# Optimization experiments

Hardware: AMD Instinct MI355X
Metric: run time of the kernel (lower is better)

## Reference

```python
import jax, jax.numpy as jnp
import numpy as np

HEADS = 8
DIM_HEAD = 64
QUERY_DIM = 512
CONTEXT_DIM = 512
OUT_DIM = 512
INNER = HEADS * DIM_HEAD  # 512


def setup_inputs() -> dict:
    key = jax.random.key(0)
    ks = jax.random.split(key, 6)
    B, N, S, M = 2, 1024, 4, 2048
    x = jax.random.normal(ks[0], (B, N, S, QUERY_DIM), dtype=jnp.float32)
    context = jax.random.normal(ks[1], (B, M, CONTEXT_DIM), dtype=jnp.float32)
    # Linear weights stored as [in, out] so y = x @ W (matches torch Linear with W.T)
    Wq = jax.random.normal(ks[2], (QUERY_DIM, INNER), dtype=jnp.float32) / np.sqrt(QUERY_DIM)
    Wkv = jax.random.normal(ks[3], (CONTEXT_DIM, 2 * INNER), dtype=jnp.float32) / np.sqrt(CONTEXT_DIM)
    Wo = jax.random.normal(ks[4], (INNER, OUT_DIM), dtype=jnp.float32) / np.sqrt(INNER)
    bo = jax.random.normal(ks[5], (OUT_DIM,), dtype=jnp.float32) * 0.01
    return {"x": x, "context": context, "Wq": Wq, "Wkv": Wkv, "Wo": Wo, "bo": bo}


def reference(x, context, Wq, Wkv, Wo, bo):
    B, N, S, _ = x.shape
    M = context.shape[1]
    scale = DIM_HEAD ** -0.5
    # projections
    q = (x @ Wq).reshape(B, N, S, HEADS, DIM_HEAD)            # b n s h d
    kv = context @ Wkv                                        # b m (2*inner)
    k, v = jnp.split(kv, 2, axis=-1)
    k = k.reshape(B, M, HEADS, DIM_HEAD)                      # b m h d
    v = v.reshape(B, M, HEADS, DIM_HEAD)
    # attention scores: [(b h) s n m] expressed as bhsnm
    sim = jnp.einsum('bnshd,bmhd->bhsnm', q, k) * scale
    attn = jax.nn.softmax(sim, axis=-1)
    out = jnp.einsum('bhsnm,bmhd->bnshd', attn, v)            # b n s h d
    out = out.reshape(B, N, S, INNER)
    return out @ Wo + bo
```

## Files before the change

kernel.cpp:

```cpp
#include <hip/hip_runtime.h>

typedef __bf16 bf16;
typedef __bf16 bf16x8 __attribute__((ext_vector_type(8)));
typedef __bf16 bf16x4 __attribute__((ext_vector_type(4)));
typedef float f32x4 __attribute__((ext_vector_type(4)));

#define SCL 0.18033688011112042f

#define GLOAD_LDS16(g, l)                                          \
  __builtin_amdgcn_global_load_lds(                                \
      (const __attribute__((address_space(1))) void*)(g),          \
      (__attribute__((address_space(3))) void*)(l), 16, 0, 0)

__global__ __launch_bounds__(256) void convert_bf16(const float* __restrict__ x,
                                                    const float* __restrict__ ctx,
                                                    bf16* __restrict__ xb,
                                                    bf16* __restrict__ cb) {
  const int bid = blockIdx.x;
  const float* src;
  bf16* dst;
  size_t off;
  if (bid < 2048) { src = x; dst = xb; off = (size_t)bid * 2048; }
  else            { src = ctx; dst = cb; off = (size_t)(bid - 2048) * 2048; }
  size_t i = off + (size_t)threadIdx.x * 8;
  float4 a0 = *(const float4*)&src[i];
  float4 a1 = *(const float4*)&src[i + 4];
  bf16x8 o;
  o[0] = (bf16)a0.x; o[1] = (bf16)a0.y; o[2] = (bf16)a0.z; o[3] = (bf16)a0.w;
  o[4] = (bf16)a1.x; o[5] = (bf16)a1.y; o[6] = (bf16)a1.z; o[7] = (bf16)a1.w;
  *(bf16x8*)&dst[i] = o;
}

__global__ __launch_bounds__(256) void transpose_all(const float* __restrict__ Wq,
                                                     const float* __restrict__ Wkv,
                                                     const float* __restrict__ Wo,
                                                     bf16* __restrict__ Wqt,
                                                     bf16* __restrict__ Wkvt,
                                                     bf16* __restrict__ Wot) {
  __shared__ float tile[32][33];
  const int bx = blockIdx.x;
  const float* W; bf16* Wt; int N, n0;
  if (bx < 16)      { W = Wq;  Wt = Wqt;  N = 512;  n0 = bx * 32; }
  else if (bx < 48) { W = Wkv; Wt = Wkvt; N = 1024; n0 = (bx - 16) * 32; }
  else              { W = Wo;  Wt = Wot;  N = 512;  n0 = (bx - 48) * 32; }
  const int K = 512;
  const int tid = threadIdx.x;
  const int j = tid & 31, i0 = tid >> 5;
  const int k0 = blockIdx.y * 32;
#pragma unroll
  for (int ii = 0; ii < 4; ii++) {
    int i = i0 * 4 + ii;
    tile[i][j] = W[(size_t)(k0 + i) * N + n0 + j];
  }
  __syncthreads();
#pragma unroll
  for (int ii = 0; ii < 4; ii++) {
    int i = i0 * 4 + ii;
    Wt[(size_t)(n0 + i) * K + k0 + j] = (bf16)tile[j][i];
  }
}

template <int MODE>
__global__ __launch_bounds__(256) void gemm128(const bf16* __restrict__ A,
                                               const bf16* __restrict__ Bt,
                                               void* __restrict__ Cout,
                                               const float* __restrict__ bias,
                                               bf16* __restrict__ Vtb,
                                               int M, int N, int K) {
  const int tid = threadIdx.x;
  const int wave = tid >> 6, lane = tid & 63;
  const int quad = lane >> 4, l15 = lane & 15;
  const int m0 = blockIdx.y * 128, n0 = blockIdx.x * 128;

  __shared__ __align__(16) bf16 As[128 * 64];
  __shared__ __align__(16) bf16 Bs[128 * 64];

  f32x4 acc[4][4] = {};

  const int srow8 = lane >> 3, schunk = lane & 7;
  const int gchunk = schunk ^ srow8;
  const bf16* Ag = A + (size_t)(m0 + wave * 8 + srow8) * K + gchunk * 8;
  const bf16* Bg = Bt + (size_t)(n0 + wave * 8 + srow8) * K + gchunk * 8;
  bf16* Asw = &As[wave * 8 * 64];
  bf16* Bsw = &Bs[wave * 8 * 64];

  const int mrow = (wave & 1) * 64, ncol = (wave >> 1) * 64;

  for (int kt = 0; kt < K; kt += 64) {
#pragma unroll
    for (int r = 0; r < 4; r++) {
      GLOAD_LDS16(Ag + kt + (size_t)(r * 32) * K, Asw + r * 32 * 64);
      GLOAD_LDS16(Bg + kt + (size_t)(r * 32) * K, Bsw + r * 32 * 64);
    }
    __syncthreads();
#pragma unroll
    for (int h = 0; h < 2; h++) {
      bf16x8 af[4], bfr[4];
#pragma unroll
      for (int i = 0; i < 4; i++) {
        int R = mrow + i * 16 + l15;
        af[i] = *(const bf16x8*)&As[R * 64 + (((h * 4 + quad) ^ (R & 7)) * 8)];
      }
#pragma unroll
      for (int j = 0; j < 4; j++) {
        int R = ncol + j * 16 + l15;
        bfr[j] = *(const bf16x8*)&Bs[R * 64 + (((h * 4 + quad) ^ (R & 7)) * 8)];
      }
#pragma unroll
      for (int i = 0; i < 4; i++)
#pragma unroll
        for (int j = 0; j < 4; j++)
          acc[i][j] = __builtin_amdgcn_mfma_f32_16x16x32_bf16(af[i], bfr[j], acc[i][j], 0, 0, 0);
    }
    __syncthreads();
  }

#pragma unroll
  for (int i = 0; i < 4; i++) {
    const int row = m0 + mrow + i * 16 + quad * 4;
#pragma unroll
    for (int j = 0; j < 4; j++) {
      const int col = n0 + ncol + j * 16 + l15;
      if constexpr (MODE == 0) {
        bf16* C = (bf16*)Cout;
#pragma unroll
        for (int r = 0; r < 4; r++)
          C[(size_t)(row + r) * N + col] = (bf16)(acc[i][j][r] * SCL);
      } else if constexpr (MODE == 1) {
        if (col < 512) {
          bf16* Kb = (bf16*)Cout;
#pragma unroll
          for (int r = 0; r < 4; r++)
            Kb[(size_t)(row + r) * 512 + col] = (bf16)acc[i][j][r];
        } else {
          const int hh = (col - 512) >> 6, d = (col - 512) & 63;
          const int bb = row >> 11, mb = row & 2047;
          bf16x4 pk;
          pk[0] = (bf16)acc[i][j][0]; pk[1] = (bf16)acc[i][j][1];
          pk[2] = (bf16)acc[i][j][2]; pk[3] = (bf16)acc[i][j][3];
          *(bf16x4*)&Vtb[((size_t)(bb * 8 + hh) * 64 + d) * 2048 + mb] = pk;
        }
      } else {
        float* C = (float*)Cout;
        const float bv = bias[col];
#pragma unroll
        for (int r = 0; r < 4; r++)
          C[(size_t)(row + r) * N + col] = acc[i][j][r] + bv;
      }
    }
  }
}

__global__ __launch_bounds__(256) void attn_kernel(const bf16* __restrict__ q,
                                                   const bf16* __restrict__ Kb,
                                                   const bf16* __restrict__ Vtb,
                                                   bf16* __restrict__ attn_out) {
  const int tid = threadIdx.x;
  const int wave = tid >> 6, lane = tid & 63;
  const int quad = lane >> 4, l15 = lane & 15;
  const int bid = blockIdx.x;
  const int nt = bid & 15, h = (bid >> 4) & 7, s = (bid >> 7) & 3, b = bid >> 9;
  const int n0 = nt * 64;

  __shared__ __align__(16) bf16 Kl[2][64 * 64];
  __shared__ __align__(16) bf16 Vl[2][64 * 64];
  __shared__ __align__(16) bf16 Pl[4][16 * 64];
  bf16* Pw = &Pl[wave][0];

  const int nrow = n0 + wave * 16 + l15;
  const size_t qoff = ((size_t)((b * 1024 + nrow) * 4 + s)) * 512 + h * 64;
  const bf16x8 qf0 = *(const bf16x8*)&q[qoff + quad * 8];
  const bf16x8 qf1 = *(const bf16x8*)&q[qoff + 32 + quad * 8];

  float l_part = 0.0f;
  f32x4 o[4] = {};

  const int srow = tid >> 2, c0 = tid & 3;
  const bf16* Kg = Kb + (size_t)(b * 2048 + srow) * 512 + h * 64 + c0 * 16;
  const bf16* Vg = Vtb + ((size_t)(b * 8 + h) * 64 + srow) * 2048 + c0 * 16;
  const int ssw = srow & 7;
  const int koff0 = srow * 64 + ((c0 * 2) ^ ssw) * 8;
  const int koff1 = srow * 64 + ((c0 * 2 + 1) ^ ssw) * 8;

  uint4 kr0 = *(const uint4*)Kg;
  uint4 kr1 = *(const uint4*)(Kg + 8);
  uint4 vr0 = *(const uint4*)Vg;
  uint4 vr1 = *(const uint4*)(Vg + 8);
  *(uint4*)&Kl[0][koff0] = kr0; *(uint4*)&Kl[0][koff1] = kr1;
  *(uint4*)&Vl[0][koff0] = vr0; *(uint4*)&Vl[0][koff1] = vr1;

  const int psw = l15 & 7;

  for (int t = 0; t < 32; ++t) {
    __syncthreads();
    if (t < 31) {
      const bf16* kg = Kg + (size_t)(t + 1) * 64 * 512;
      const bf16* vg = Vg + (t + 1) * 64;
      kr0 = *(const uint4*)kg; kr1 = *(const uint4*)(kg + 8);
      vr0 = *(const uint4*)vg; vr1 = *(const uint4*)(vg + 8);
    }
    const bf16* Kc = &Kl[t & 1][0];
    const bf16* Vc = &Vl[t & 1][0];

    f32x4 sf[4];
#pragma unroll
    for (int mc = 0; mc < 4; mc++) {
      f32x4 z = {};
      bf16x8 kf0 = *(const bf16x8*)&Kc[(mc * 16 + l15) * 64 + ((quad ^ psw) * 8)];
      bf16x8 kf1 = *(const bf16x8*)&Kc[(mc * 16 + l15) * 64 + (((4 + quad) ^ psw) * 8)];
      z = __builtin_amdgcn_mfma_f32_16x16x32_bf16(kf0, qf0, z, 0, 0, 0);
      z = __builtin_amdgcn_mfma_f32_16x16x32_bf16(kf1, qf1, z, 0, 0, 0);
      sf[mc] = z;
    }

    float p[4][4];
#pragma unroll
    for (int mc = 0; mc < 4; mc++)
#pragma unroll
      for (int r = 0; r < 4; r++) {
        p[mc][r] = __builtin_amdgcn_exp2f(sf[mc][r]);
        l_part += p[mc][r];
      }

#pragma unroll
    for (int mc = 0; mc < 4; mc++) {
      bf16x4 pk;
      pk[0] = (bf16)p[mc][0]; pk[1] = (bf16)p[mc][1];
      pk[2] = (bf16)p[mc][2]; pk[3] = (bf16)p[mc][3];
      *(bf16x4*)&Pw[l15 * 64 + (((mc * 2 + (quad >> 1)) ^ psw)) * 8 + (quad & 1) * 4] = pk;
    }

#pragma unroll
    for (int mch = 0; mch < 2; mch++) {
      bf16x8 pf = *(const bf16x8*)&Pw[l15 * 64 + (((mch * 4 + quad) ^ psw)) * 8];
#pragma unroll
      for (int dg = 0; dg < 4; dg++) {
        bf16x8 vf = *(const bf16x8*)&Vc[(dg * 16 + l15) * 64 + (((mch * 4 + quad) ^ psw)) * 8];
        o[dg] = __builtin_amdgcn_mfma_f32_16x16x32_bf16(vf, pf, o[dg], 0, 0, 0);
      }
    }

    if (t < 31) {
      bf16* Kn = &Kl[(t + 1) & 1][0];
      bf16* Vn = &Vl[(t + 1) & 1][0];
      *(uint4*)&Kn[koff0] = kr0; *(uint4*)&Kn[koff1] = kr1;
      *(uint4*)&Vn[koff0] = vr0; *(uint4*)&Vn[koff1] = vr1;
    }
  }

  l_part += __shfl_xor(l_part, 16);
  l_part += __shfl_xor(l_part, 32);
  const float inv = 1.0f / l_part;
#pragma unroll
  for (int dg = 0; dg < 4; dg++) {
    bf16x4 ok;
    ok[0] = (bf16)(o[dg][0] * inv); ok[1] = (bf16)(o[dg][1] * inv);
    ok[2] = (bf16)(o[dg][2] * inv); ok[3] = (bf16)(o[dg][3] * inv);
    *(bf16x4*)&attn_out[qoff + dg * 16 + quad * 4] = ok;
  }
}

extern "C" void kernel_launch(void* const* d_in, const int* in_sizes, int n_in,
                              void* d_out, int out_size, void* d_ws, size_t ws_size,
                              hipStream_t stream) {
  const float* x = (const float*)d_in[0];
  const float* context = (const float*)d_in[1];
  const float* Wq = (const float*)d_in[2];
  const float* Wkv = (const float*)d_in[3];
  const float* Wo = (const float*)d_in[4];
  const float* bo = (const float*)d_in[5];
  float* out = (float*)d_out;

  char* ws = (char*)d_ws;
  bf16* xb   = (bf16*)(ws);
  bf16* cb   = (bf16*)(ws + (8u << 20));
  bf16* qb   = (bf16*)(ws + (12u << 20));
  bf16* Kb   = (bf16*)(ws + (20u << 20));
  bf16* Vtb  = (bf16*)(ws + (24u << 20));
  bf16* Wqt  = (bf16*)(ws + (28u << 20));
  bf16* Wkvt = (bf16*)(ws + (28u << 20) + 524288);
  bf16* Wot  = (bf16*)(ws + (28u << 20) + 1572864);
  bf16* attn = xb;

  convert_bf16<<<3072, 256, 0, stream>>>(x, context, xb, cb);
  transpose_all<<<dim3(64, 16), 256, 0, stream>>>(Wq, Wkv, Wo, Wqt, Wkvt, Wot);

  gemm128<0><<<dim3(4, 64), 256, 0, stream>>>(xb, Wqt, qb, nullptr, nullptr, 8192, 512, 512);
  gemm128<1><<<dim3(8, 32), 256, 0, stream>>>(cb, Wkvt, Kb, nullptr, Vtb, 4096, 1024, 512);
  attn_kernel<<<1024, 256, 0, stream>>>(qb, Kb, Vtb, attn);
  gemm128<2><<<dim3(4, 64), 256, 0, stream>>>(attn, Wot, out, bo, nullptr, 8192, 512, 512);
}
```

Measured before the change: 182.7 us.

## Merge prep and projection kernels, shrink GEMM tiles, load V directly to registers

New measurement: 243.6 us. 1.33x slower.

```diff
diff --git a/kernel.cpp b/kernel.cpp
--- a/kernel.cpp
+++ b/kernel.cpp
@@ -12,149 +12,168 @@
       (const __attribute__((address_space(1))) void*)(g),          \
       (__attribute__((address_space(3))) void*)(l), 16, 0, 0)
 
-__global__ __launch_bounds__(256) void convert_bf16(const float* __restrict__ x,
-                                                    const float* __restrict__ ctx,
-                                                    bf16* __restrict__ xb,
-                                                    bf16* __restrict__ cb) {
+__global__ __launch_bounds__(256) void prep_kernel(const float* __restrict__ x,
+                                                   const float* __restrict__ ctx,
+                                                   const float* __restrict__ Wq,
+                                                   const float* __restrict__ Wkv,
+                                                   const float* __restrict__ Wo,
+                                                   bf16* __restrict__ xb,
+                                                   bf16* __restrict__ cb,
+                                                   bf16* __restrict__ Wqt,
+                                                   bf16* __restrict__ Wkvt,
+                                                   bf16* __restrict__ Wot) {
   const int bid = blockIdx.x;
-  const float* src;
-  bf16* dst;
-  size_t off;
-  if (bid < 2048) { src = x; dst = xb; off = (size_t)bid * 2048; }
-  else            { src = ctx; dst = cb; off = (size_t)(bid - 2048) * 2048; }
-  size_t i = off + (size_t)threadIdx.x * 8;
-  float4 a0 = *(const float4*)&src[i];
-  float4 a1 = *(const float4*)&src[i + 4];
-  bf16x8 o;
-  o[0] = (bf16)a0.x; o[1] = (bf16)a0.y; o[2] = (bf16)a0.z; o[3] = (bf16)a0.w;
-  o[4] = (bf16)a1.x; o[5] = (bf16)a1.y; o[6] = (bf16)a1.z; o[7] = (bf16)a1.w;
-  *(bf16x8*)&dst[i] = o;
-}
-
-__global__ __launch_bounds__(256) void transpose_all(const float* __restrict__ Wq,
-                                                     const float* __restrict__ Wkv,
-                                                     const float* __restrict__ Wo,
-                                                     bf16* __restrict__ Wqt,
-                                                     bf16* __restrict__ Wkvt,
-                                                     bf16* __restrict__ Wot) {
-  __shared__ float tile[32][33];
-  const int bx = blockIdx.x;
-  const float* W; bf16* Wt; int N, n0;
-  if (bx < 16)      { W = Wq;  Wt = Wqt;  N = 512;  n0 = bx * 32; }
-  else if (bx < 48) { W = Wkv; Wt = Wkvt; N = 1024; n0 = (bx - 16) * 32; }
-  else              { W = Wo;  Wt = Wot;  N = 512;  n0 = (bx - 48) * 32; }
-  const int K = 512;
   const int tid = threadIdx.x;
-  const int j = tid & 31, i0 = tid >> 5;
-  const int k0 = blockIdx.y * 32;
-#pragma unroll
-  for (int ii = 0; ii < 4; ii++) {
-    int i = i0 * 4 + ii;
-    tile[i][j] = W[(size_t)(k0 + i) * N + n0 + j];
-  }
-  __syncthreads();
-#pragma unroll
-  for (int ii = 0; ii < 4; ii++) {
-    int i = i0 * 4 + ii;
-    Wt[(size_t)(n0 + i) * K + k0 + j] = (bf16)tile[j][i];
-  }
-}
-
-template <int MODE>
-__global__ __launch_bounds__(256) void gemm128(const bf16* __restrict__ A,
-                                               const bf16* __restrict__ Bt,
-                                               void* __restrict__ Cout,
-                                               const float* __restrict__ bias,
-                                               bf16* __restrict__ Vtb,
-                                               int M, int N, int K) {
+  if (bid < 3072) {
+    const float* src;
+    bf16* dst;
+    size_t off;
+    if (bid < 2048) { src = x; dst = xb; off = (size_t)bid * 2048; }
+    else            { src = ctx; dst = cb; off = (size_t)(bid - 2048) * 2048; }
+    size_t i = off + (size_t)tid * 8;
+    float4 a0 = *(const float4*)&src[i];
+    float4 a1 = *(const float4*)&src[i + 4];
+    bf16x8 o;
+    o[0] = (bf16)a0.x; o[1] = (bf16)a0.y; o[2] = (bf16)a0.z; o[3] = (bf16)a0.w;
+    o[4] = (bf16)a1.x; o[5] = (bf16)a1.y; o[6] = (bf16)a1.z; o[7] = (bf16)a1.w;
+    *(bf16x8*)&dst[i] = o;
+  } else {
+    __shared__ float tile[32][33];
+    const int idx = bid - 3072;
+    const int bx = idx & 63;
+    const int k0 = (idx >> 6) * 32;
+    const float* W; bf16* Wt; int N, n0;
+    if (bx < 16)      { W = Wq;  Wt = Wqt;  N = 512;  n0 = bx * 32; }
+    else if (bx < 48) { W = Wkv; Wt = Wkvt; N = 1024; n0 = (bx - 16) * 32; }
+    else              { W = Wo;  Wt = Wot;  N = 512;  n0 = (bx - 48) * 32; }
+    const int j = tid & 31, i0 = tid >> 5;
+#pragma unroll
+    for (int ii = 0; ii < 4; ii++) {
+      int i = i0 * 4 + ii;
+      tile[i][j] = W[(size_t)(k0 + i) * N + n0 + j];
+    }
+    __syncthreads();
+#pragma unroll
+    for (int ii = 0; ii < 4; ii++) {
+      int i = i0 * 4 + ii;
+      Wt[(size_t)(n0 + i) * 512 + k0 + j] = (bf16)tile[j][i];
+    }
+  }
+}
+
+__device__ __forceinline__ void gemm64_core(const bf16* __restrict__ A,
+                                            const bf16* __restrict__ Bt,
+                                            int m0, int n0,
+                                            bf16* As, bf16* Bs,
+                                            f32x4 (&acc)[4],
+                                            int wave, int lane) {
+  const int l15 = lane & 15, quad = lane >> 4;
+  const int lrow = lane >> 3;
+  const int gchunk = (lane & 7) ^ lrow;
+  const bf16* Ag = A + (size_t)(m0 + wave * 8 + lrow) * 512 + gchunk * 8;
+  const bf16* Bg = Bt + (size_t)(n0 + wave * 8 + lrow) * 512 + gchunk * 8;
+  bf16* Asw = As + wave * 8 * 64;
+  bf16* Bsw = Bs + wave * 8 * 64;
+
+  for (int kt = 0; kt < 512; kt += 64) {
+    GLOAD_LDS16(Ag + kt, Asw);
+    GLOAD_LDS16(Ag + kt + (size_t)32 * 512, Asw + 32 * 64);
+    GLOAD_LDS16(Bg + kt, Bsw);
+    GLOAD_LDS16(Bg + kt + (size_t)32 * 512, Bsw + 32 * 64);
+    __syncthreads();
+#pragma unroll
+    for (int h = 0; h < 2; h++) {
+      const int R = wave * 16 + l15;
+      bf16x8 af = *(const bf16x8*)&As[R * 64 + (((h * 4 + quad) ^ (R & 7)) * 8)];
+#pragma unroll
+      for (int g = 0; g < 4; g++) {
+        const int Rb = g * 16 + l15;
+        bf16x8 bf = *(const bf16x8*)&Bs[Rb * 64 + (((h * 4 + quad) ^ (Rb & 7)) * 8)];
+        acc[g] = __builtin_amdgcn_mfma_f32_16x16x32_bf16(af, bf, acc[g], 0, 0, 0);
+      }
+    }
+    __syncthreads();
+  }
+}
+
+__global__ __launch_bounds__(256) void proj_kernel(const bf16* __restrict__ xb,
+                                                   const bf16* __restrict__ cb,
+                                                   const bf16* __restrict__ Wqt,
+                                                   const bf16* __restrict__ Wkvt,
+                                                   bf16* __restrict__ qb,
+                                                   bf16* __restrict__ Kb,
+                                                   bf16* __restrict__ Vtb) {
+  __shared__ __align__(16) bf16 As[64 * 64];
+  __shared__ __align__(16) bf16 Bs[64 * 64];
   const int tid = threadIdx.x;
   const int wave = tid >> 6, lane = tid & 63;
   const int quad = lane >> 4, l15 = lane & 15;
-  const int m0 = blockIdx.y * 128, n0 = blockIdx.x * 128;
-
-  __shared__ __align__(16) bf16 As[128 * 64];
-  __shared__ __align__(16) bf16 Bs[128 * 64];
-
-  f32x4 acc[4][4] = {};
-
-  const int srow8 = lane >> 3, schunk = lane & 7;
-  const int gchunk = schunk ^ srow8;
-  const bf16* Ag = A + (size_t)(m0 + wave * 8 + srow8) * K + gchunk * 8;
-  const bf16* Bg = Bt + (size_t)(n0 + wave * 8 + srow8) * K + gchunk * 8;
-  bf16* Asw = &As[wave * 8 * 64];
-  bf16* Bsw = &Bs[wave * 8 * 64];
-
-  const int mrow = (wave & 1) * 64, ncol = (wave >> 1) * 64;
-
-  for (int kt = 0; kt < K; kt += 64) {
-#pragma unroll
-    for (int r = 0; r < 4; r++) {
-      GLOAD_LDS16(Ag + kt + (size_t)(r * 32) * K, Asw + r * 32 * 64);
-      GLOAD_LDS16(Bg + kt + (size_t)(r * 32) * K, Bsw + r * 32 * 64);
-    }
-    __syncthreads();
-#pragma unroll
-    for (int h = 0; h < 2; h++) {
-      bf16x8 af[4], bfr[4];
-#pragma unroll
-      for (int i = 0; i < 4; i++) {
-        int R = mrow + i * 16 + l15;
-        af[i] = *(const bf16x8*)&As[R * 64 + (((h * 4 + quad) ^ (R & 7)) * 8)];
+  const int bid = blockIdx.x;
+  f32x4 acc[4] = {};
+
+  if (bid < 1024) {
+    const int m0 = (bid >> 3) * 64, n0 = (bid & 7) * 64;
+    gemm64_core(xb, Wqt, m0, n0, As, Bs, acc, wave, lane);
+    const int rowb = m0 + wave * 16 + quad * 4;
+#pragma unroll
+    for (int g = 0; g < 4; g++) {
+      const int col = n0 + g * 16 + l15;
+#pragma unroll
+      for (int r = 0; r < 4; r++)
+        qb[(size_t)(rowb + r) * 512 + col] = (bf16)(acc[g][r] * SCL);
+    }
+  } else {
+    const int idx = bid - 1024;
+    const int m0 = (idx >> 4) * 64, n0 = (idx & 15) * 64;
+    gemm64_core(cb, Wkvt, m0, n0, As, Bs, acc, wave, lane);
+    const int rowb = m0 + wave * 16 + quad * 4;
+#pragma unroll
+    for (int g = 0; g < 4; g++) {
+      const int col = n0 + g * 16 + l15;
+      if (col < 512) {
+#pragma unroll
+        for (int r = 0; r < 4; r++)
+          Kb[(size_t)(rowb + r) * 512 + col] = (bf16)acc[g][r];
+      } else {
+        const int hh = (col - 512) >> 6, d = (col - 512) & 63;
+        const int bb = rowb >> 11, mb = rowb & 2047;
+        bf16x4 pk;
+        pk[0] = (bf16)acc[g][0]; pk[1] = (bf16)acc[g][1];
+        pk[2] = (bf16)acc[g][2]; pk[3] = (bf16)acc[g][3];
+        *(bf16x4*)&Vtb[((size_t)(bb * 8 + hh) * 64 + d) * 2048 + mb] = pk;
       }
-#pragma unroll
-      for (int j = 0; j < 4; j++) {
-        int R = ncol + j * 16 + l15;
-        bfr[j] = *(const bf16x8*)&Bs[R * 64 + (((h * 4 + quad) ^ (R & 7)) * 8)];
-      }
-#pragma unroll
-      for (int i = 0; i < 4; i++)
-#pragma unroll
-        for (int j = 0; j < 4; j++)
-          acc[i][j] = __builtin_amdgcn_mfma_f32_16x16x32_bf16(af[i], bfr[j], acc[i][j], 0, 0, 0);
-    }
-    __syncthreads();
-  }
-
-#pragma unroll
-  for (int i = 0; i < 4; i++) {
-    const int row = m0 + mrow + i * 16 + quad * 4;
-#pragma unroll
-    for (int j = 0; j < 4; j++) {
-      const int col = n0 + ncol + j * 16 + l15;
-      if constexpr (MODE == 0) {
-        bf16* C = (bf16*)Cout;
-#pragma unroll
-        for (int r = 0; r < 4; r++)
-          C[(size_t)(row + r) * N + col] = (bf16)(acc[i][j][r] * SCL);
-      } else if constexpr (MODE == 1) {
-        if (col < 512) {
-          bf16* Kb = (bf16*)Cout;
-#pragma unroll
-          for (int r = 0; r < 4; r++)
-            Kb[(size_t)(row + r) * 512 + col] = (bf16)acc[i][j][r];
-        } else {
-          const int hh = (col - 512) >> 6, d = (col - 512) & 63;
-          const int bb = row >> 11, mb = row & 2047;
-          bf16x4 pk;
-          pk[0] = (bf16)acc[i][j][0]; pk[1] = (bf16)acc[i][j][1];
-          pk[2] = (bf16)acc[i][j][2]; pk[3] = (bf16)acc[i][j][3];
-          *(bf16x4*)&Vtb[((size_t)(bb * 8 + hh) * 64 + d) * 2048 + mb] = pk;
-        }
-      } else {
-        float* C = (float*)Cout;
-        const float bv = bias[col];
-#pragma unroll
-        for (int r = 0; r < 4; r++)
-          C[(size_t)(row + r) * N + col] = acc[i][j][r] + bv;
-      }
-    }
-  }
-}
-
-__global__ __launch_bounds__(256) void attn_kernel(const bf16* __restrict__ q,
-                                                   const bf16* __restrict__ Kb,
-                                                   const bf16* __restrict__ Vtb,
-                                                   bf16* __restrict__ attn_out) {
+    }
+  }
+}
+
+__global__ __launch_bounds__(256) void outproj_kernel(const bf16* __restrict__ attn,
+                                                      const bf16* __restrict__ Wot,
+                                                      float* __restrict__ out,
+                                                      const float* __restrict__ bias) {
+  __shared__ __align__(16) bf16 As[64 * 64];
+  __shared__ __align__(16) bf16 Bs[64 * 64];
+  const int tid = threadIdx.x;
+  const int wave = tid >> 6, lane = tid & 63;
+  const int quad = lane >> 4, l15 = lane & 15;
+  const int bid = blockIdx.x;
+  const int m0 = (bid >> 3) * 64, n0 = (bid & 7) * 64;
+  f32x4 acc[4] = {};
+  gemm64_core(attn, Wot, m0, n0, As, Bs, acc, wave, lane);
+  const int rowb = m0 + wave * 16 + quad * 4;
+#pragma unroll
+  for (int g = 0; g < 4; g++) {
+    const int col = n0 + g * 16 + l15;
+    const float bv = bias[col];
+#pragma unroll
+    for (int r = 0; r < 4; r++)
+      out[(size_t)(rowb + r) * 512 + col] = acc[g][r] + bv;
+  }
+}
+
+__global__ __launch_bounds__(256, 4) void attn_kernel(const bf16* __restrict__ q,
+                                                      const bf16* __restrict__ Kb,
+                                                      const bf16* __restrict__ Vtb,
+                                                      bf16* __restrict__ attn_out) {
   const int tid = threadIdx.x;
   const int wave = tid >> 6, lane = tid & 63;
   const int quad = lane >> 4, l15 = lane & 15;
@@ -163,7 +182,6 @@
   const int n0 = nt * 64;
 
   __shared__ __align__(16) bf16 Kl[2][64 * 64];
-  __shared__ __align__(16) bf16 Vl[2][64 * 64];
   __shared__ __align__(16) bf16 Pl[4][16 * 64];
   bf16* Pw = &Pl[wave][0];
 
@@ -177,30 +195,39 @@
 
   const int srow = tid >> 2, c0 = tid & 3;
   const bf16* Kg = Kb + (size_t)(b * 2048 + srow) * 512 + h * 64 + c0 * 16;
-  const bf16* Vg = Vtb + ((size_t)(b * 8 + h) * 64 + srow) * 2048 + c0 * 16;
   const int ssw = srow & 7;
   const int koff0 = srow * 64 + ((c0 * 2) ^ ssw) * 8;
   const int koff1 = srow * 64 + ((c0 * 2 + 1) ^ ssw) * 8;
 
+  const bf16* vp[4];
+#pragma unroll
+  for (int dg = 0; dg < 4; dg++)
+    vp[dg] = Vtb + ((size_t)(b * 8 + h) * 64 + dg * 16 + l15) * 2048 + quad * 8;
+
   uint4 kr0 = *(const uint4*)Kg;
   uint4 kr1 = *(const uint4*)(Kg + 8);
-  uint4 vr0 = *(const uint4*)Vg;
-  uint4 vr1 = *(const uint4*)(Vg + 8);
-  *(uint4*)&Kl[0][koff0] = kr0; *(uint4*)&Kl[0][koff1] = kr1;
-  *(uint4*)&Vl[0][koff0] = vr0; *(uint4*)&Vl[0][koff1] = vr1;
+  *(uint4*)&Kl[0][koff0] = kr0;
+  *(uint4*)&Kl[0][koff1] = kr1;
 
   const int psw = l15 & 7;
 
   for (int t = 0; t < 32; ++t) {
     __syncthreads();
+
+    bf16x8 vf[4][2];
+#pragma unroll
+    for (int dg = 0; dg < 4; dg++) {
+#pragma unroll
+      for (int mch = 0; mch < 2; mch++)
+        vf[dg][mch] = *(const bf16x8*)(vp[dg] + t * 64 + mch * 32);
+    }
+
     if (t < 31) {
       const bf16* kg = Kg + (size_t)(t + 1) * 64 * 512;
-      const bf16* vg = Vg + (t + 1) * 64;
-      kr0 = *(const uint4*)kg; kr1 = *(const uint4*)(kg + 8);
-      vr0 = *(const uint4*)vg; vr1 = *(const uint4*)(vg + 8);
+      kr0 = *(const uint4*)kg;
+      kr1 = *(const uint4*)(kg + 8);
     }
     const bf16* Kc = &Kl[t & 1][0];
-    const bf16* Vc = &Vl[t & 1][0];
 
     f32x4 sf[4];
 #pragma unroll
@@ -234,17 +261,14 @@
     for (int mch = 0; mch < 2; mch++) {
       bf16x8 pf = *(const bf16x8*)&Pw[l15 * 64 + (((mch * 4 + quad) ^ psw)) * 8];
 #pragma unroll
-      for (int dg = 0; dg < 4; dg++) {
-        bf16x8 vf = *(const bf16x8*)&Vc[(dg * 16 + l15) * 64 + (((mch * 4 + quad) ^ psw)) * 8];
-        o[dg] = __builtin_amdgcn_mfma_f32_16x16x32_bf16(vf, pf, o[dg], 0, 0, 0);
-      }
+      for (int dg = 0; dg < 4; dg++)
+        o[dg] = __builtin_amdgcn_mfma_f32_16x16x32_bf16(vf[dg][mch], pf, o[dg], 0, 0, 0);
     }
 
     if (t < 31) {
       bf16* Kn = &Kl[(t + 1) & 1][0];
-      bf16* Vn = &Vl[(t + 1) & 1][0];
-      *(uint4*)&Kn[koff0] = kr0; *(uint4*)&Kn[koff1] = kr1;
-      *(uint4*)&Vn[koff0] = vr0; *(uint4*)&Vn[koff1] = vr1;
+      *(uint4*)&Kn[koff0] = kr0;
+      *(uint4*)&Kn[koff1] = kr1;
     }
   }
 
@@ -282,11 +306,8 @@
   bf16* Wot  = (bf16*)(ws + (28u << 20) + 1572864);
   bf16* attn = xb;
 
-  convert_bf16<<<3072, 256, 0, stream>>>(x, context, xb, cb);
-  transpose_all<<<dim3(64, 16), 256, 0, stream>>>(Wq, Wkv, Wo, Wqt, Wkvt, Wot);
-
-  gemm128<0><<<dim3(4, 64), 256, 0, stream>>>(xb, Wqt, qb, nullptr, nullptr, 8192, 512, 512);
-  gemm128<1><<<dim3(8, 32), 256, 0, stream>>>(cb, Wkvt, Kb, nullptr, Vtb, 4096, 1024, 512);
+  prep_kernel<<<4096, 256, 0, stream>>>(x, context, Wq, Wkv, Wo, xb, cb, Wqt, Wkvt, Wot);
+  proj_kernel<<<2048, 256, 0, stream>>>(xb, cb, Wqt, Wkvt, qb, Kb, Vtb);
   attn_kernel<<<1024, 256, 0, stream>>>(qb, Kb, Vtb, attn);
-  gemm128<2><<<dim3(4, 64), 256, 0, stream>>>(attn, Wot, out, bo, nullptr, 8192, 512, 512);
-}
+  outproj_kernel<<<1024, 256, 0, stream>>>(attn, Wot, out, bo);
+}
```
